# Optimization experiments

Hardware: AMD Instinct MI355X
Metric: run time of the kernel (lower is better)

## Reference

```python
import jax, jax.numpy as jnp
import numpy as np

DN = ('NCHW', 'OIHW', 'NCHW')  # conv dimension numbers


def conv2d_same(x, w, b=None):
    y = jax.lax.conv_general_dilated(x, w, window_strides=(1, 1), padding='SAME',
                                     dimension_numbers=DN)
    if b is not None:
        y = y + b[None, :, None, None]
    return y


def setup_inputs() -> dict:
    key = jax.random.key(0)
    k_x, k_wx, k_bx, k_wh = jax.random.split(key, 4)
    B, C_in, T, H, W = 4, 16, 64, 64, 64
    hid = 32
    kk = 3
    x = jax.random.normal(k_x, (B, C_in, T, H, W), dtype=jnp.float32)
    Wx = jax.random.normal(k_wx, (3 * hid, C_in, kk, kk), dtype=jnp.float32) * 0.1
    bx = jax.random.normal(k_bx, (3 * hid,), dtype=jnp.float32) * 0.1
    Wh = jax.random.normal(k_wh, (3 * hid, hid, kk, kk), dtype=jnp.float32) * 0.1
    return {"x": x, "Wx": Wx, "bx": bx, "Wh": Wh}


def reference(x, Wx, bx, Wh):
    # x: (B, C_in, T, H, W) -> time-major (T, B, C_in, H, W)
    B, C, T, H, W = x.shape
    hid = Wh.shape[1]
    xt = jnp.transpose(x, (2, 0, 1, 3, 4))  # (T, B, C, H, W)
    # conv_x applied outside the time loop (as in the torch code), batched over T
    x_proj = conv2d_same(xt.reshape(T * B, C, H, W), Wx, bx).reshape(T, B, 3 * hid, H, W)

    h0 = jnp.zeros((B, hid, H, W), dtype=x.dtype)

    def step(h, xp):
        g = xp + conv2d_same(h, Wh)          # (B, 3*hid, H, W)
        z, r, n = jnp.split(g, 3, axis=1)
        z = jax.nn.sigmoid(z)
        # r = sigmoid(r) is computed in the original but never used
        n = jnp.tanh(n)
        h_new = (1.0 - z) * h + z * n
        return h_new, None

    h_final, _ = jax.lax.scan(step, h0, x_proj)
    return h_final  # (B, hid, H, W)
```

## Files before the change

### kernel.cpp

```cpp
#include <hip/hip_runtime.h>
#include <math.h>


typedef _Float16 half8 __attribute__((ext_vector_type(8)));
typedef float floatx16 __attribute__((ext_vector_type(16)));

#define NROWS 144
#define RSTRIDE 136
#define LDS_DW ((NROWS * RSTRIDE + 16) / 4)

static __device__ __forceinline__ unsigned pack2(float a, float b) {
    _Float16 ha = (_Float16)a, hb = (_Float16)b;
    unsigned short ua = *(unsigned short*)&ha, ub = *(unsigned short*)&hb;
    return (unsigned)ua | ((unsigned)ub << 16);
}

__global__ __launch_bounds__(64) void build_wfrag(
    const float* __restrict__ Wx, const float* __restrict__ Wh,
    uint4* __restrict__ wfrag)
{
    const int bid   = blockIdx.x;
    const int mtile = bid / 36, chunk = bid % 36;
    const int lane  = threadIdx.x;
    const int m     = lane & 31;
    const int grow  = (m < 16) ? (mtile * 16 + m) : (64 + mtile * 16 + (m - 16));
    unsigned short h[8];
    for (int j = 0; j < 8; ++j) {
        int k   = chunk * 16 + (lane >> 5) * 8 + j;
        int cin = k / 12, t12 = k - cin * 12;
        int p = t12 >> 1, o = t12 & 1;
        int ky = p >> 1, q = p & 1;
        int kx = q ? (2 + o) : o;
        float w = 0.0f;
        if (!(q && o)) {
            if (cin < 16) w = Wx[((size_t)grow * 16 + cin) * 9 + ky * 3 + kx];
            else          w = Wh[((size_t)grow * 32 + (cin - 16)) * 9 + ky * 3 + kx];
        }
        _Float16 hw = (_Float16)w;
        h[j] = *(unsigned short*)&hw;
    }
    uint4 o4;
    o4.x = (unsigned)h[0] | ((unsigned)h[1] << 16);
    o4.y = (unsigned)h[2] | ((unsigned)h[3] << 16);
    o4.z = (unsigned)h[4] | ((unsigned)h[5] << 16);
    o4.w = (unsigned)h[6] | ((unsigned)h[7] << 16);
    wfrag[(size_t)bid * 64 + lane] = o4;
}

__global__ __launch_bounds__(256, 1) void convgru_step(
    const float* __restrict__ x, const float* __restrict__ bx,
    const uint4* __restrict__ wfrag,
    const float* __restrict__ hsrc, float* __restrict__ hdst, int t)
{
    __shared__ unsigned int plds[LDS_DW];
    const int tx = threadIdx.x;
    const int y  = blockIdx.x;
    const int b  = blockIdx.y;

    if (tx < NROWS) {
        plds[tx * 34]      = 0u;
        plds[tx * 34 + 33] = 0u;
    }
    #pragma unroll
    for (int i = 0; i < 9; ++i) {
        int task = i * 256 + tx;
        int rr   = task >> 4;
        int qd   = task & 15;
        int cin  = rr / 3;
        int ky   = rr - cin * 3;
        int ys   = y + ky - 1;
        float4 v = make_float4(0.f, 0.f, 0.f, 0.f);
        if ((unsigned)ys < 64u) {
            const float* src = (cin < 16)
                ? x + (((size_t)(b * 16 + cin) * 64 + t) * 4096)
                : hsrc + ((size_t)(b * 32 + (cin - 16)) * 4096);
            v = *(const float4*)(src + ys * 64 + qd * 4);
        }
        plds[rr * 34 + 2 * qd + 1] = pack2(v.x, v.y);
        plds[rr * 34 + 2 * qd + 2] = pack2(v.z, v.w);
    }
    __syncthreads();

    const int lane  = tx & 63;
    const int wv    = tx >> 6;
    const int mtile = wv & 1;
    const int ntile = wv >> 1;
    const int xpx   = ntile * 32 + (lane & 31);
    const int half  = lane >> 5;
    const bool par  = (xpx & 1) != 0;
    const int basev = ((2 * xpx + 2) & ~3) + half * (2 * RSTRIDE);
    const char* lb  = (const char*)plds + basev;

    floatx16 acc;
    #pragma unroll
    for (int i = 0; i < 16; ++i) acc[i] = 0.0f;

    #pragma unroll
    for (int c = 0; c < 36; ++c) {
        uint4 aw = wfrag[(size_t)((mtile * 36 + c) * 64 + lane)];
        const int B0 = c * 4 * RSTRIDE;
        unsigned d0 = *(const unsigned*)(lb + B0);
        unsigned d1 = *(const unsigned*)(lb + B0 + 4);
        unsigned d2 = *(const unsigned*)(lb + B0 + 8);
        unsigned e0 = *(const unsigned*)(lb + B0 + RSTRIDE);
        unsigned e1 = *(const unsigned*)(lb + B0 + RSTRIDE + 4);
        unsigned e2 = *(const unsigned*)(lb + B0 + RSTRIDE + 8);
        uint4 bf;
        bf.x = par ? d0 : ((d0 >> 16) | (d1 << 16));
        bf.y = par ? d1 : ((d1 >> 16) | (d2 << 16));
        bf.z = par ? e0 : ((e0 >> 16) | (e1 << 16));
        bf.w = par ? e1 : ((e1 >> 16) | (e2 << 16));
        union { uint4 u; half8 h; } ua, ub;
        ua.u = aw; ub.u = bf;
        acc = __builtin_amdgcn_mfma_f32_32x32x16_f16(ua.h, ub.h, acc, 0, 0, 0);
    }

    #pragma unroll
    for (int r = 0; r < 8; ++r) {
        const int row = (r & 3) + 8 * (r >> 2) + 4 * half;
        const int oc  = mtile * 16 + row;
        const size_t a = (size_t)(b * 32 + oc) * 4096 + y * 64 + xpx;
        float zp = acc[r]     + bx[oc];
        float np = acc[r + 8] + bx[64 + oc];
        float hp = hsrc[a];
        float z  = 1.0f / (1.0f + __expf(-zp));
        float e  = __expf(2.0f * np);
        float n  = 1.0f - 2.0f / (e + 1.0f);
        hdst[a] = (1.0f - z) * hp + z * n;
    }
}

extern "C" void kernel_launch(void* const* d_in, const int* in_sizes, int n_in,
                              void* d_out, int out_size, void* d_ws, size_t ws_size,
                              hipStream_t stream) {
    const float* x  = (const float*)d_in[0];
    const float* Wx = (const float*)d_in[1];
    const float* bx = (const float*)d_in[2];
    const float* Wh = (const float*)d_in[3];
    float* out = (float*)d_out;
    float* hws = (float*)d_ws;
    uint4* wfrag = (uint4*)((char*)d_ws + (4u << 20));

    hipMemsetAsync(d_out, 0, (size_t)524288 * sizeof(float), stream);
    hipLaunchKernelGGL(build_wfrag, dim3(72), dim3(64), 0, stream, Wx, Wh, wfrag);

    dim3 grid(64, 4), block(256);
    for (int t = 0; t < 64; ++t) {
        const float* src = (t & 1) ? hws : out;
        float*       dst = (t & 1) ? out : hws;
        hipLaunchKernelGGL(convgru_step, grid, block, 0, stream,
                           x, bx, wfrag, src, dst, t);
    }
}
```

Baseline: 695.5 us.

## Split K across wave pairs and store two pre-shifted LDS copies

Doubles the block to 512 threads so each output tile's K loop is split between two waves, with partial accumulators reduced through LDS before the gate epilogue. The input patch is written into LDS twice, once per pixel-parity alignment, so the MFMA operand loads become aligned dword reads instead of shift-and-merge. The previous hidden state is prefetched before the MFMA loop. The costs are more LDS, an extra barrier and reduction, and half the waves sitting idle during the epilogue.

```diff
diff --git a/kernel.cpp b/kernel.cpp
--- a/kernel.cpp
+++ b/kernel.cpp
@@ -5,9 +5,10 @@
 typedef _Float16 half8 __attribute__((ext_vector_type(8)));
 typedef float floatx16 __attribute__((ext_vector_type(16)));
 
-#define NROWS 144
-#define RSTRIDE 136
-#define LDS_DW ((NROWS * RSTRIDE + 16) / 4)
+#define RS 144
+#define CP1 (144 * RS)
+#define SCRDW (2 * 144 * RS / 4)
+#define LDS_DW (SCRDW + 4 * 16 * 68)
 
 static __device__ __forceinline__ unsigned pack2(float a, float b) {
     _Float16 ha = (_Float16)a, hb = (_Float16)b;
@@ -47,86 +48,113 @@
     wfrag[(size_t)bid * 64 + lane] = o4;
 }
 
-__global__ __launch_bounds__(256, 1) void convgru_step(
+__global__ __launch_bounds__(512, 1) void convgru_step(
     const float* __restrict__ x, const float* __restrict__ bx,
     const uint4* __restrict__ wfrag,
     const float* __restrict__ hsrc, float* __restrict__ hdst, int t)
 {
-    __shared__ unsigned int plds[LDS_DW];
+    __shared__ unsigned plds[LDS_DW];
     const int tx = threadIdx.x;
     const int y  = blockIdx.x;
     const int b  = blockIdx.y;
 
-    if (tx < NROWS) {
-        plds[tx * 34]      = 0u;
-        plds[tx * 34 + 33] = 0u;
-    }
+    if (tx < 144) plds[tx * 36 + 34] = 0u;
+
     #pragma unroll
-    for (int i = 0; i < 9; ++i) {
-        int task = i * 256 + tx;
-        int rr   = task >> 4;
-        int qd   = task & 15;
-        int cin  = rr / 3;
-        int ky   = rr - cin * 3;
-        int ys   = y + ky - 1;
-        float4 v = make_float4(0.f, 0.f, 0.f, 0.f);
-        if ((unsigned)ys < 64u) {
-            const float* src = (cin < 16)
-                ? x + (((size_t)(b * 16 + cin) * 64 + t) * 4096)
-                : hsrc + ((size_t)(b * 32 + (cin - 16)) * 4096);
-            v = *(const float4*)(src + ys * 64 + qd * 4);
+    for (int i = 0; i < 5; ++i) {
+        int task = i * 512 + tx;
+        if (task < 2304) {
+            int rr  = task >> 4;
+            int g   = task & 15;
+            int cin = rr / 3;
+            int ky  = rr - cin * 3;
+            int ys  = y + ky - 1;
+            float4 v = make_float4(0.f, 0.f, 0.f, 0.f);
+            if ((unsigned)ys < 64u) {
+                const float* src = (cin < 16)
+                    ? x + (((size_t)(b * 16 + cin) * 64 + t) * 4096)
+                    : hsrc + ((size_t)(b * 32 + (cin - 16)) * 4096);
+                v = *(const float4*)(src + ys * 64 + g * 4);
+            }
+            float prev = __shfl_up(v.w, 1);
+            if (g == 0) prev = 0.0f;
+            const int r36 = rr * 36;
+            plds[r36 + 2 * g + 2] = pack2(v.x, v.y);
+            plds[r36 + 2 * g + 3] = pack2(v.z, v.w);
+            plds[CP1 / 4 + r36 + 2 * g]     = pack2(prev, v.x);
+            plds[CP1 / 4 + r36 + 2 * g + 1] = pack2(v.y, v.z);
+            if (g == 15)
+                plds[CP1 / 4 + r36 + 32] = pack2(v.w, 0.0f);
         }
-        plds[rr * 34 + 2 * qd + 1] = pack2(v.x, v.y);
-        plds[rr * 34 + 2 * qd + 2] = pack2(v.z, v.w);
     }
     __syncthreads();
 
     const int lane  = tx & 63;
     const int wv    = tx >> 6;
-    const int mtile = wv & 1;
-    const int ntile = wv >> 1;
+    const int kh    = wv & 1;
+    const int mtile = (wv >> 1) & 1;
+    const int ntile = wv >> 2;
+    const int tile  = wv >> 1;
     const int xpx   = ntile * 32 + (lane & 31);
     const int half  = lane >> 5;
-    const bool par  = (xpx & 1) != 0;
-    const int basev = ((2 * xpx + 2) & ~3) + half * (2 * RSTRIDE);
-    const char* lb  = (const char*)plds + basev;
+    const int lb_off = ((xpx & 1) ? (2 * xpx + 6) : (CP1 + 2 * xpx))
+                       + half * (2 * RS);
+    const char* lbase = (const char*)plds + lb_off;
+
+    float hprev[8];
+    if (kh == 0) {
+        #pragma unroll
+        for (int r = 0; r < 8; ++r) {
+            const int row = (r & 3) + 8 * (r >> 2) + 4 * half;
+            const int oc  = mtile * 16 + row;
+            hprev[r] = hsrc[(size_t)(b * 32 + oc) * 4096 + y * 64 + xpx];
+        }
+    }
 
     floatx16 acc;
     #pragma unroll
     for (int i = 0; i < 16; ++i) acc[i] = 0.0f;
 
+    const int c0 = kh * 18;
     #pragma unroll
-    for (int c = 0; c < 36; ++c) {
+    for (int j = 0; j < 18; ++j) {
+        const int c = c0 + j;
         uint4 aw = wfrag[(size_t)((mtile * 36 + c) * 64 + lane)];
-        const int B0 = c * 4 * RSTRIDE;
-        unsigned d0 = *(const unsigned*)(lb + B0);
-        unsigned d1 = *(const unsigned*)(lb + B0 + 4);
-        unsigned d2 = *(const unsigned*)(lb + B0 + 8);
-        unsigned e0 = *(const unsigned*)(lb + B0 + RSTRIDE);
-        unsigned e1 = *(const unsigned*)(lb + B0 + RSTRIDE + 4);
-        unsigned e2 = *(const unsigned*)(lb + B0 + RSTRIDE + 8);
-        uint4 bf;
-        bf.x = par ? d0 : ((d0 >> 16) | (d1 << 16));
-        bf.y = par ? d1 : ((d1 >> 16) | (d2 << 16));
-        bf.z = par ? e0 : ((e0 >> 16) | (e1 << 16));
-        bf.w = par ? e1 : ((e1 >> 16) | (e2 << 16));
+        const int B0 = c * 4 * RS;
+        unsigned d0 = *(const unsigned*)(lbase + B0);
+        unsigned d1 = *(const unsigned*)(lbase + B0 + 4);
+        unsigned e0 = *(const unsigned*)(lbase + B0 + RS);
+        unsigned e1 = *(const unsigned*)(lbase + B0 + RS + 4);
+        uint4 bf; bf.x = d0; bf.y = d1; bf.z = e0; bf.w = e1;
         union { uint4 u; half8 h; } ua, ub;
         ua.u = aw; ub.u = bf;
         acc = __builtin_amdgcn_mfma_f32_32x32x16_f16(ua.h, ub.h, acc, 0, 0, 0);
     }
 
-    #pragma unroll
-    for (int r = 0; r < 8; ++r) {
-        const int row = (r & 3) + 8 * (r >> 2) + 4 * half;
-        const int oc  = mtile * 16 + row;
-        const size_t a = (size_t)(b * 32 + oc) * 4096 + y * 64 + xpx;
-        float zp = acc[r]     + bx[oc];
-        float np = acc[r + 8] + bx[64 + oc];
-        float hp = hsrc[a];
-        float z  = 1.0f / (1.0f + __expf(-zp));
-        float e  = __expf(2.0f * np);
-        float n  = 1.0f - 2.0f / (e + 1.0f);
-        hdst[a] = (1.0f - z) * hp + z * n;
+    if (kh == 1) {
+        #pragma unroll
+        for (int r = 0; r < 16; ++r)
+            plds[SCRDW + tile * 1088 + r * 68 + lane] = __float_as_uint(acc[r]);
+    }
+    __syncthreads();
+
+    if (kh == 0) {
+        #pragma unroll
+        for (int r = 0; r < 16; ++r)
+            acc[r] += __uint_as_float(plds[SCRDW + tile * 1088 + r * 68 + lane]);
+
+        #pragma unroll
+        for (int r = 0; r < 8; ++r) {
+            const int row = (r & 3) + 8 * (r >> 2) + 4 * half;
+            const int oc  = mtile * 16 + row;
+            const size_t a = (size_t)(b * 32 + oc) * 4096 + y * 64 + xpx;
+            float zp = acc[r]     + bx[oc];
+            float np = acc[r + 8] + bx[64 + oc];
+            float z  = 1.0f / (1.0f + __expf(-zp));
+            float e  = __expf(2.0f * np);
+            float n  = 1.0f - 2.0f / (e + 1.0f);
+            hdst[a] = (1.0f - z) * hprev[r] + z * n;
+        }
     }
 }
 
@@ -144,7 +172,7 @@
     hipMemsetAsync(d_out, 0, (size_t)524288 * sizeof(float), stream);
     hipLaunchKernelGGL(build_wfrag, dim3(72), dim3(64), 0, stream, Wx, Wh, wfrag);
 
-    dim3 grid(64, 4), block(256);
+    dim3 grid(64, 4), block(512);
     for (int t = 0; t < 64; ++t) {
         const float* src = (t & 1) ? hws : out;
         float*       dst = (t & 1) ? out : hws;
```

Result: faster. 641.9 us (-7.7%).

## Fuse two GRU timesteps per launch using halo recomputation in LDS

Applied to the files above, without the earlier changes.

Each launch now computes two consecutive timesteps. It loads a 5-row halo of h and x(t), then recomputes the intermediate hidden state for rows y-1..y+1 into LDS in fp16 and uses it for the second step. Block size doubles to 512 threads, the second-step GEMM is split across K halves with an LDS reduction, and the bias is staged in LDS. This halves the kernel launch count and the global round-trips of h, at the cost of roughly 1.5x the first-step MFMA work plus an extra fp16 rounding of the intermediate state.

```diff
diff --git a/kernel.cpp b/kernel.cpp
--- a/kernel.cpp
+++ b/kernel.cpp
@@ -5,14 +5,76 @@
 typedef _Float16 half8 __attribute__((ext_vector_type(8)));
 typedef float floatx16 __attribute__((ext_vector_type(16)));
 
-#define NROWS 144
-#define RSTRIDE 136
-#define LDS_DW ((NROWS * RSTRIDE + 16) / 4)
+#define RSB 136
+#define BLK 34
+#define PA_DW 0
+#define PX1_DW 5440
+#define PX2_DW 8160
+#define PB_DW 9792
+#define BX_DW 13056
+#define LDS_DW 13152
+#define PA_B (PA_DW * 4)
+#define PX1_B (PX1_DW * 4)
+#define PX2_B (PX2_DW * 4)
+#define PB_B (PB_DW * 4)
 
 static __device__ __forceinline__ unsigned pack2(float a, float b) {
     _Float16 ha = (_Float16)a, hb = (_Float16)b;
     unsigned short ua = *(unsigned short*)&ha, ub = *(unsigned short*)&hb;
     return (unsigned)ua | ((unsigned)ub << 16);
+}
+
+static __device__ __forceinline__ float gru_update(float zp, float np, float hp) {
+    float z = 1.0f / (1.0f + __expf(-zp));
+    float e = __expf(2.0f * np);
+    float n = 1.0f - 2.0f / (e + 1.0f);
+    return (1.0f - z) * hp + z * n;
+}
+
+static __device__ __forceinline__ int krow_off(int c, int s, int dyterm,
+                                               int xbase, int xnr,
+                                               int hbase, int hnr, int bias)
+{
+    int rr = 4 * c + s;
+    int off;
+    if (rr < 48) { int cin = rr / 3, ky = rr - cin * 3;
+                   off = xbase + (cin * xnr + bias + ky) * RSB; }
+    else         { int r2 = rr - 48; int cin = r2 / 3, ky = r2 - cin * 3;
+                   off = hbase + (cin * hnr + bias + ky) * RSB; }
+    return off + dyterm;
+}
+
+static __device__ __forceinline__ floatx16 gemm_range(
+    const unsigned* plds, const uint4* wfrag,
+    int c0, int c1, int mt, int lane, int half, bool par,
+    const char* lbase, int dyterm,
+    int xbase, int xnr, int hbase, int hnr, int bias, floatx16 acc)
+{
+#pragma unroll
+    for (int c = c0; c < c1; ++c) {
+        uint4 aw = wfrag[(size_t)(mt * 36 + c) * 64 + lane];
+        int o0 = krow_off(c, 0, dyterm, xbase, xnr, hbase, hnr, bias);
+        int o1 = krow_off(c, 1, dyterm, xbase, xnr, hbase, hnr, bias);
+        int o2 = krow_off(c, 2, dyterm, xbase, xnr, hbase, hnr, bias);
+        int o3 = krow_off(c, 3, dyterm, xbase, xnr, hbase, hnr, bias);
+        int offA = half ? o2 : o0;
+        int offB = half ? o3 : o1;
+        unsigned d0 = *(const unsigned*)(lbase + offA);
+        unsigned d1 = *(const unsigned*)(lbase + offA + 4);
+        unsigned d2 = *(const unsigned*)(lbase + offA + 8);
+        unsigned e0 = *(const unsigned*)(lbase + offB);
+        unsigned e1 = *(const unsigned*)(lbase + offB + 4);
+        unsigned e2 = *(const unsigned*)(lbase + offB + 8);
+        uint4 bf;
+        bf.x = par ? d0 : ((d0 >> 16) | (d1 << 16));
+        bf.y = par ? d1 : ((d1 >> 16) | (d2 << 16));
+        bf.z = par ? e0 : ((e0 >> 16) | (e1 << 16));
+        bf.w = par ? e1 : ((e1 >> 16) | (e2 << 16));
+        union { uint4 u; half8 h; } ua, ub;
+        ua.u = aw; ub.u = bf;
+        acc = __builtin_amdgcn_mfma_f32_32x32x16_f16(ua.h, ub.h, acc, 0, 0, 0);
+    }
+    return acc;
 }
 
 __global__ __launch_bounds__(64) void build_wfrag(
@@ -47,86 +109,122 @@
     wfrag[(size_t)bid * 64 + lane] = o4;
 }
 
-__global__ __launch_bounds__(256, 1) void convgru_step(
+__global__ __launch_bounds__(512, 1) void convgru_2step(
     const float* __restrict__ x, const float* __restrict__ bx,
     const uint4* __restrict__ wfrag,
-    const float* __restrict__ hsrc, float* __restrict__ hdst, int t)
-{
-    __shared__ unsigned int plds[LDS_DW];
+    const float* __restrict__ hsrc, float* __restrict__ hdst, int t0)
+{
+    __shared__ unsigned plds[LDS_DW];
     const int tx = threadIdx.x;
     const int y  = blockIdx.x;
     const int b  = blockIdx.y;
 
-    if (tx < NROWS) {
-        plds[tx * 34]      = 0u;
-        plds[tx * 34 + 33] = 0u;
-    }
-    #pragma unroll
+#pragma unroll
+    for (int i = 0; i < 8; ++i) {
+        int z = i * 512 + tx;
+        if (z < 3264) plds[PB_DW + z] = 0u;
+        else if (z < 3840) {
+            int rb = z - 3264;
+            int blkid = rb >> 1;
+            plds[blkid * BLK + ((rb & 1) ? 33 : 0)] = 0u;
+        }
+        else if (z < 3936) plds[BX_DW + (z - 3840)] = __float_as_uint(bx[z - 3840]);
+    }
+
+#pragma unroll
     for (int i = 0; i < 9; ++i) {
-        int task = i * 256 + tx;
-        int rr   = task >> 4;
-        int qd   = task & 15;
-        int cin  = rr / 3;
-        int ky   = rr - cin * 3;
-        int ys   = y + ky - 1;
+        int task = i * 512 + tx;
+        int g = task & 15, idx = task >> 4;
+        const float* src; int ys;
+        if (idx < 160) {
+            int cin = idx / 5, iy = idx - cin * 5;
+            ys = y - 2 + iy;
+            src = hsrc + (size_t)(b * 32 + cin) * 4096;
+        } else if (idx < 240) {
+            int r2 = idx - 160; int cin = r2 / 5, iy = r2 - cin * 5;
+            ys = y - 2 + iy;
+            src = x + ((size_t)(b * 16 + cin) * 64 + t0) * 4096;
+        } else {
+            int r2 = idx - 240; int cin = r2 / 3, iy = r2 - cin * 3;
+            ys = y - 1 + iy;
+            src = x + ((size_t)(b * 16 + cin) * 64 + t0 + 1) * 4096;
+        }
         float4 v = make_float4(0.f, 0.f, 0.f, 0.f);
-        if ((unsigned)ys < 64u) {
-            const float* src = (cin < 16)
-                ? x + (((size_t)(b * 16 + cin) * 64 + t) * 4096)
-                : hsrc + ((size_t)(b * 32 + (cin - 16)) * 4096);
-            v = *(const float4*)(src + ys * 64 + qd * 4);
-        }
-        plds[rr * 34 + 2 * qd + 1] = pack2(v.x, v.y);
-        plds[rr * 34 + 2 * qd + 2] = pack2(v.z, v.w);
+        if ((unsigned)ys < 64u) v = *(const float4*)(src + ys * 64 + g * 4);
+        plds[idx * BLK + 2 * g + 1] = pack2(v.x, v.y);
+        plds[idx * BLK + 2 * g + 2] = pack2(v.z, v.w);
     }
     __syncthreads();
 
-    const int lane  = tx & 63;
-    const int wv    = tx >> 6;
-    const int mtile = wv & 1;
-    const int ntile = wv >> 1;
-    const int xpx   = ntile * 32 + (lane & 31);
-    const int half  = lane >> 5;
-    const bool par  = (xpx & 1) != 0;
-    const int basev = ((2 * xpx + 2) & ~3) + half * (2 * RSTRIDE);
-    const char* lb  = (const char*)plds + basev;
-
-    floatx16 acc;
-    #pragma unroll
-    for (int i = 0; i < 16; ++i) acc[i] = 0.0f;
-
-    #pragma unroll
-    for (int c = 0; c < 36; ++c) {
-        uint4 aw = wfrag[(size_t)((mtile * 36 + c) * 64 + lane)];
-        const int B0 = c * 4 * RSTRIDE;
-        unsigned d0 = *(const unsigned*)(lb + B0);
-        unsigned d1 = *(const unsigned*)(lb + B0 + 4);
-        unsigned d2 = *(const unsigned*)(lb + B0 + 8);
-        unsigned e0 = *(const unsigned*)(lb + B0 + RSTRIDE);
-        unsigned e1 = *(const unsigned*)(lb + B0 + RSTRIDE + 4);
-        unsigned e2 = *(const unsigned*)(lb + B0 + RSTRIDE + 8);
-        uint4 bf;
-        bf.x = par ? d0 : ((d0 >> 16) | (d1 << 16));
-        bf.y = par ? d1 : ((d1 >> 16) | (d2 << 16));
-        bf.z = par ? e0 : ((e0 >> 16) | (e1 << 16));
-        bf.w = par ? e1 : ((e1 >> 16) | (e2 << 16));
-        union { uint4 u; half8 h; } ua, ub;
-        ua.u = aw; ub.u = bf;
-        acc = __builtin_amdgcn_mfma_f32_32x32x16_f16(ua.h, ub.h, acc, 0, 0, 0);
-    }
-
-    #pragma unroll
-    for (int r = 0; r < 8; ++r) {
-        const int row = (r & 3) + 8 * (r >> 2) + 4 * half;
-        const int oc  = mtile * 16 + row;
-        const size_t a = (size_t)(b * 32 + oc) * 4096 + y * 64 + xpx;
-        float zp = acc[r]     + bx[oc];
-        float np = acc[r + 8] + bx[64 + oc];
-        float hp = hsrc[a];
-        float z  = 1.0f / (1.0f + __expf(-zp));
-        float e  = __expf(2.0f * np);
-        float n  = 1.0f - 2.0f / (e + 1.0f);
-        hdst[a] = (1.0f - z) * hp + z * n;
+    const int lane = tx & 63, wv = tx >> 6, half = lane >> 5;
+
+    for (int ti = wv; ti < 12; ti += 8) {
+        const int mt  = ti & 1;
+        const int dy  = ((ti >> 1) % 3) - 1;
+        const int chf = ti / 6;
+        const int yp  = y + dy;
+        if ((unsigned)yp < 64u) {
+            const int xpx = chf * 32 + (lane & 31);
+            const bool par = (xpx & 1) != 0;
+            const char* lbase = (const char*)plds + ((2 * xpx + 2) & ~3);
+            floatx16 acc;
+            #pragma unroll
+            for (int i2 = 0; i2 < 16; ++i2) acc[i2] = 0.f;
+            acc = gemm_range(plds, wfrag, 0, 36, mt, lane, half, par, lbase,
+                             dy * RSB, PX1_B, 5, PA_B, 5, 1, acc);
+            #pragma unroll
+            for (int r = 0; r < 8; ++r) {
+                const int row = (r & 3) + 8 * (r >> 2) + 4 * half;
+                const int oc  = mt * 16 + row;
+                const float bz = __uint_as_float(plds[BX_DW + oc]);
+                const float bn = __uint_as_float(plds[BX_DW + 64 + oc]);
+                const float hp = hsrc[(size_t)(b * 32 + oc) * 4096 + yp * 64 + xpx];
+                float hn = gru_update(acc[r] + bz, acc[r + 8] + bn, hp);
+                _Float16 hf = (_Float16)hn;
+                *(unsigned short*)((char*)plds + PB_B + (oc * 3 + dy + 1) * RSB
+                                   + 2 * xpx + 4) = *(unsigned short*)&hf;
+            }
+        }
+    }
+    __syncthreads();
+
+    {
+        const int kh = wv & 1, tile = wv >> 1;
+        const int mt = tile & 1, chf = tile >> 1;
+        const int xpx = chf * 32 + (lane & 31);
+        const bool par = (xpx & 1) != 0;
+        const char* lbase = (const char*)plds + ((2 * xpx + 2) & ~3);
+        floatx16 acc;
+        #pragma unroll
+        for (int i2 = 0; i2 < 16; ++i2) acc[i2] = 0.f;
+        if (kh == 0) {
+            acc = gemm_range(plds, wfrag, 0, 18, mt, lane, half, par, lbase,
+                             0, PX2_B, 3, PB_B, 3, 0, acc);
+        } else {
+            acc = gemm_range(plds, wfrag, 18, 36, mt, lane, half, par, lbase,
+                             0, PX2_B, 3, PB_B, 3, 0, acc);
+            #pragma unroll
+            for (int r = 0; r < 16; ++r)
+                plds[PA_DW + tile * 1088 + r * 68 + lane] = __float_as_uint(acc[r]);
+        }
+        __syncthreads();
+        if (kh == 0) {
+            #pragma unroll
+            for (int r = 0; r < 16; ++r)
+                acc[r] += __uint_as_float(plds[PA_DW + tile * 1088 + r * 68 + lane]);
+            #pragma unroll
+            for (int r = 0; r < 8; ++r) {
+                const int row = (r & 3) + 8 * (r >> 2) + 4 * half;
+                const int oc  = mt * 16 + row;
+                const float bz = __uint_as_float(plds[BX_DW + oc]);
+                const float bn = __uint_as_float(plds[BX_DW + 64 + oc]);
+                union { unsigned short u; _Float16 f; } hu;
+                hu.u = *(const unsigned short*)((const char*)plds + PB_B
+                        + (oc * 3 + 1) * RSB + 2 * xpx + 4);
+                float hn = gru_update(acc[r] + bz, acc[r + 8] + bn, (float)hu.f);
+                hdst[(size_t)(b * 32 + oc) * 4096 + y * 64 + xpx] = hn;
+            }
+        }
     }
 }
 
@@ -144,11 +242,11 @@
     hipMemsetAsync(d_out, 0, (size_t)524288 * sizeof(float), stream);
     hipLaunchKernelGGL(build_wfrag, dim3(72), dim3(64), 0, stream, Wx, Wh, wfrag);
 
-    dim3 grid(64, 4), block(256);
-    for (int t = 0; t < 64; ++t) {
-        const float* src = (t & 1) ? hws : out;
-        float*       dst = (t & 1) ? out : hws;
-        hipLaunchKernelGGL(convgru_step, grid, block, 0, stream,
-                           x, bx, wfrag, src, dst, t);
-    }
-}
+    dim3 grid(64, 4), block(512);
+    for (int s = 0; s < 32; ++s) {
+        const float* src = (s & 1) ? hws : out;
+        float*       dst = (s & 1) ? out : hws;
+        hipLaunchKernelGGL(convgru_2step, grid, block, 0, stream,
+                           x, bx, wfrag, src, dst, 2 * s);
+    }
+}
```

Measured after the change: 729.9 us. 4.9% more time.
